# Performance work log

Measured on AMD Instinct MI355X. Metric: run time of the kernel, lower is better.

The kernel has to match this reference:

```python
import jax, jax.numpy as jnp
import numpy as np

N_QUBITS = 8
N_LAYERS = 2
DIM = 2 ** N_QUBITS  # 256


def _ry(theta):
    h = theta * 0.5
    c, s = jnp.cos(h), jnp.sin(h)
    return jnp.stack([jnp.stack([c, -s]), jnp.stack([s, c])]).astype(jnp.complex64)


def _rz(theta):
    e = jnp.exp(-0.5j * theta.astype(jnp.complex64))
    z = jnp.zeros((), jnp.complex64)
    return jnp.stack([jnp.stack([e, z]), jnp.stack([z, jnp.conj(e)])])


def _apply_1q(state, U, w):
    # state: (2,)*n tensor, wire 0 = most significant (PennyLane convention)
    s = jnp.moveaxis(state, w, 0)
    s = jnp.tensordot(U, s, axes=((1,), (0,)))
    return jnp.moveaxis(s, 0, w)


def _cnot(state, c, t):
    s = jnp.moveaxis(state, (c, t), (0, 1))
    s = jnp.stack([s[0, 0], s[0, 1], s[1, 1], s[1, 0]]).reshape((2, 2) + s.shape[2:])
    return jnp.moveaxis(s, (0, 1), (c, t))


def _conv_pair(state, q1, q2, p):
    state = _apply_1q(state, _ry(p[0]), q1)
    state = _apply_1q(state, _ry(p[1]), q2)
    state = _cnot(state, q1, q2)
    state = _apply_1q(state, _ry(p[2]), q1)
    state = _apply_1q(state, _ry(p[3]), q2)
    state = _cnot(state, q2, q1)
    return state


def _circuit(angles, node_idx, adj, qp):
    n = N_QUBITS
    state = jnp.zeros((2,) * n, jnp.complex64).at[(0,) * n].set(1.0)
    a = jnp.clip(angles, -np.pi, np.pi)
    # angle encoding: RY on all wires, RZ on wires 0..n/2-1
    for i in range(n):
        state = _apply_1q(state, _ry(a[i]), i)
    for i in range(n // 2):
        state = _apply_1q(state, _rz(a[i + n // 2]), i)
    # graph-structure entanglement: conditional CNOT(c=node%n, t) if adj[c,t]>0
    c = (node_idx % n).astype(jnp.int32)
    adj_row = adj[c]
    flat = state.reshape(-1)
    idx = jnp.arange(DIM, dtype=jnp.int32)
    bit_c = (idx >> (n - 1 - c)) & 1  # dynamic control wire
    for t in range(n):
        perm = idx ^ (bit_c << (n - 1 - t))
        cond = (adj_row[t] > 0) & (t != c)
        flat = jnp.where(cond, flat[perm], flat)
    state = flat.reshape((2,) * n)
    # quantum conv layers
    ppc = 4 * (n - 1)
    off = 0
    for _ in range(N_LAYERS):
        p = qp[off:off + ppc]
        k = 0
        for i in range(0, n - 1, 2):
            state = _conv_pair(state, i, i + 1, p[k:k + 4]); k += 4
        for i in range(1, n - 1, 2):
            state = _conv_pair(state, i, i + 1, p[k:k + 4]); k += 4
        off += ppc
    # pooling rotations on even wires
    pool = qp[off:off + n]
    for q in range(0, n, 2):
        state = _apply_1q(state, _ry(pool[q]), q)
    # <Z_w> expectation values
    probs = jnp.abs(state) ** 2
    z = jnp.stack([probs.take(0, axis=w).sum() - probs.take(1, axis=w).sum()
                   for w in range(n)])
    return z


def setup_inputs() -> dict:
    key = jax.random.key(0)
    ks = jax.random.split(key, 12)
    B, S, N, F = 64, 12, 207, 2
    x = jax.random.normal(ks[0], (B, S, N, F), jnp.float32)
    adj = jax.random.randint(ks[1], (N, N), 0, 2).astype(jnp.float32)
    w_proj = jax.random.normal(ks[2], (N_QUBITS, S * F), jnp.float32) * 0.1
    b_proj = jax.random.normal(ks[3], (N_QUBITS,), jnp.float32) * 0.1
    q_params = jax.random.normal(ks[4], (4 * (N_QUBITS - 1) * N_LAYERS + N_QUBITS,), jnp.float32) * 0.1
    w1 = jax.random.normal(ks[5], (64, N_QUBITS), jnp.float32) * 0.1
    b1 = jax.random.normal(ks[6], (64,), jnp.float32) * 0.1
    w2 = jax.random.normal(ks[7], (32, 64), jnp.float32) * 0.1
    b2 = jax.random.normal(ks[8], (32,), jnp.float32) * 0.1
    w3 = jax.random.normal(ks[9], (1, 32), jnp.float32) * 0.1
    b3 = jax.random.normal(ks[10], (1,), jnp.float32) * 0.1
    return dict(x=x, adj=adj, w_proj=w_proj, b_proj=b_proj, q_params=q_params,
                w1=w1, b1=b1, w2=w2, b2=b2, w3=w3, b3=b3)


def reference(x, adj, w_proj, b_proj, q_params, w1, b1, w2, b2, w3, b3):
    B, S, N, F = x.shape
    feats = jnp.transpose(x, (0, 2, 1, 3)).reshape(B, N, S * F)
    angles = feats @ w_proj.T + b_proj                      # (B, N, 8)
    node_idx = jnp.tile(jnp.arange(N, dtype=jnp.int32), B)  # (B*N,)
    z = jax.vmap(_circuit, in_axes=(0, 0, None, None))(
        angles.reshape(B * N, N_QUBITS), node_idx, adj, q_params)
    # original detaches quantum features before the classical head
    z = jax.lax.stop_gradient(z).reshape(B, N, N_QUBITS).astype(jnp.float32)
    h = jax.nn.relu(z @ w1.T + b1)   # dropout is identity in eval mode
    h = jax.nn.relu(h @ w2.T + b2)
    out = h @ w3.T + b3              # (B, N, 1)
    return out.squeeze(-1)
```

## Files before the change

### kernel.cpp

```cpp
#include <hip/hip_runtime.h>
#include <math.h>

#define DEV static __device__ __forceinline__

constexpr int SS = 12;
constexpr int NN = 207;
constexpr int NCIRC = 64 * NN;


template<int M> DEV float sxc(float v) { return __shfl_xor(v, M, 64); }

#define RY0(c, s) do { float _c=(c), _s=(s), _a;                         \
    _a=r0; r0=fmaf(_c,_a,-_s*r1); r1=fmaf(_s,_a,_c*r1);                  \
    _a=r2; r2=fmaf(_c,_a,-_s*r3); r3=fmaf(_s,_a,_c*r3);                  \
    _a=i0; i0=fmaf(_c,_a,-_s*i1); i1=fmaf(_s,_a,_c*i1);                  \
    _a=i2; i2=fmaf(_c,_a,-_s*i3); i3=fmaf(_s,_a,_c*i3); } while (0)

#define RY1(c, s) do { float _c=(c), _s=(s), _a;                         \
    _a=r0; r0=fmaf(_c,_a,-_s*r2); r2=fmaf(_s,_a,_c*r2);                  \
    _a=r1; r1=fmaf(_c,_a,-_s*r3); r3=fmaf(_s,_a,_c*r3);                  \
    _a=i0; i0=fmaf(_c,_a,-_s*i2); i2=fmaf(_s,_a,_c*i2);                  \
    _a=i1; i1=fmaf(_c,_a,-_s*i3); i3=fmaf(_s,_a,_c*i3); } while (0)

#define SWAP23 do { float _t=r2; r2=r3; r3=_t; _t=i2; i2=i3; i3=_t; } while (0)
#define SWAP13 do { float _t=r1; r1=r3; r3=_t; _t=i1; i1=i3; i3=_t; } while (0)

#define CONV10(T) do { RY1((T)[0],(T)[1]); RY0((T)[2],(T)[3]); SWAP23;   \
                       RY1((T)[4],(T)[5]); RY0((T)[6],(T)[7]); SWAP13; } while (0)
#define CONV01(T) do { RY0((T)[0],(T)[1]); RY1((T)[2],(T)[3]); SWAP13;   \
                       RY0((T)[4],(T)[5]); RY1((T)[6],(T)[7]); SWAP23; } while (0)

#define SWKL1(J) do { const bool _lb = (lane >> (J)) & 1;                \
    float _t0=sxc<(1<<(J))>(r2), _t1=sxc<(1<<(J))>(r3);                  \
    float _t2=sxc<(1<<(J))>(r0), _t3=sxc<(1<<(J))>(r1);                  \
    r0=_lb?_t0:r0; r1=_lb?_t1:r1; r2=_lb?r2:_t2; r3=_lb?r3:_t3;          \
    _t0=sxc<(1<<(J))>(i2); _t1=sxc<(1<<(J))>(i3);                        \
    _t2=sxc<(1<<(J))>(i0); _t3=sxc<(1<<(J))>(i1);                        \
    i0=_lb?_t0:i0; i1=_lb?_t1:i1; i2=_lb?i2:_t2; i3=_lb?i3:_t3; } while (0)

#define SWKL0(J) do { const bool _lb = (lane >> (J)) & 1;                \
    float _t0=sxc<(1<<(J))>(r1), _t1=sxc<(1<<(J))>(r0);                  \
    float _t2=sxc<(1<<(J))>(r3), _t3=sxc<(1<<(J))>(r2);                  \
    r0=_lb?_t0:r0; r1=_lb?r1:_t1; r2=_lb?_t2:r2; r3=_lb?r3:_t3;          \
    _t0=sxc<(1<<(J))>(i1); _t1=sxc<(1<<(J))>(i0);                        \
    _t2=sxc<(1<<(J))>(i3); _t3=sxc<(1<<(J))>(i2);                        \
    i0=_lb?_t0:i0; i1=_lb?i1:_t1; i2=_lb?_t2:i2; i3=_lb?i3:_t3; } while (0)

#define RYL(J, c, s) do { float _c=(c), _s=(s);                          \
    const float _sg = ((lane >> (J)) & 1) ? _s : -_s;                    \
    float _p;                                                            \
    _p=sxc<(1<<(J))>(r0); r0=fmaf(_c,r0,_sg*_p);                         \
    _p=sxc<(1<<(J))>(r1); r1=fmaf(_c,r1,_sg*_p);                         \
    _p=sxc<(1<<(J))>(r2); r2=fmaf(_c,r2,_sg*_p);                         \
    _p=sxc<(1<<(J))>(r3); r3=fmaf(_c,r3,_sg*_p);                         \
    _p=sxc<(1<<(J))>(i0); i0=fmaf(_c,i0,_sg*_p);                         \
    _p=sxc<(1<<(J))>(i1); i1=fmaf(_c,i1,_sg*_p);                         \
    _p=sxc<(1<<(J))>(i2); i2=fmaf(_c,i2,_sg*_p);                         \
    _p=sxc<(1<<(J))>(i3); i3=fmaf(_c,i3,_sg*_p); } while (0)

__global__ void trig_kernel(const float* __restrict__ qp, float* __restrict__ tab) {
    int i = threadIdx.x;
    if (i < 64) {
        float s, c;
        sincosf(0.5f * qp[i], &s, &c);
        tab[2 * i]     = c;
        tab[2 * i + 1] = s;
    }
}

__global__ __launch_bounds__(256) void qcnn_kernel(
    const float* __restrict__ x, const float* __restrict__ adj,
    const float* __restrict__ w_proj, const float* __restrict__ b_proj,
    const float* __restrict__ tab,
    const float* __restrict__ w1, const float* __restrict__ b1,
    const float* __restrict__ w2, const float* __restrict__ b2,
    const float* __restrict__ w3, const float* __restrict__ b3,
    float* __restrict__ out)
{
    const int lane = threadIdx.x & 63;
    const int wv   = threadIdx.x >> 6;
    const int g    = blockIdx.x * 4 + wv;
    const int b    = g / NN;
    const int node = g - b * NN;

    float ang[8];
#pragma unroll
    for (int k = 0; k < 8; k++) ang[k] = b_proj[k];
    const float* xp = x + ((size_t)b * SS * NN + node) * 2;
#pragma unroll
    for (int s = 0; s < SS; s++) {
        const float2 xv = *(const float2*)(xp + (size_t)s * (NN * 2));
#pragma unroll
        for (int k = 0; k < 8; k++) {
            ang[k] = fmaf(xv.x, w_proj[k * 24 + 2 * s],     ang[k]);
            ang[k] = fmaf(xv.y, w_proj[k * 24 + 2 * s + 1], ang[k]);
        }
    }
    const float PI_F = 3.14159265358979323846f;
#pragma unroll
    for (int k = 0; k < 8; k++) ang[k] = fminf(fmaxf(ang[k], -PI_F), PI_F);

    float cc[8], ss[8];
#pragma unroll
    for (int i = 0; i < 8; i++) sincosf(0.5f * ang[i], &ss[i], &cc[i]);

    float A = 1.0f;
#pragma unroll
    for (int i = 0; i < 6; i++)
        A *= ((lane >> (5 - i)) & 1) ? ss[i] : cc[i];
    float phi = 0.0f;
#pragma unroll
    for (int i = 0; i < 4; i++)
        phi += ((lane >> (5 - i)) & 1) ? 0.5f * ang[4 + i] : -0.5f * ang[4 + i];
    float cp, sp;
    sincosf(phi, &sp, &cp);

    const float A0 = A * cc[6] * cc[7];
    const float A1 = A * cc[6] * ss[7];
    const float A2 = A * ss[6] * cc[7];
    const float A3 = A * ss[6] * ss[7];
    float r0 = A0 * cp, i0 = A0 * sp;
    float r1 = A1 * cp, i1 = A1 * sp;
    float r2 = A2 * cp, i2 = A2 * sp;
    float r3 = A3 * cp, i3 = A3 * sp;

    const int c = node & 7;
    int M = 0;
#pragma unroll
    for (int t = 0; t < 8; t++) {
        float av = adj[c * NN + t];
        if (t != c && av > 0.0f) M |= 1 << (7 - t);
    }
    if (M) {
        const int Mlane = M >> 2;
        const int Mlo   = M & 3;
        float p0r, p1r, p2r, p3r, p0i, p1i, p2i, p3i;
        if (Mlo == 0) {
            p0r = __shfl_xor(r0, Mlane, 64); p1r = __shfl_xor(r1, Mlane, 64);
            p2r = __shfl_xor(r2, Mlane, 64); p3r = __shfl_xor(r3, Mlane, 64);
            p0i = __shfl_xor(i0, Mlane, 64); p1i = __shfl_xor(i1, Mlane, 64);
            p2i = __shfl_xor(i2, Mlane, 64); p3i = __shfl_xor(i3, Mlane, 64);
        } else if (Mlo == 1) {
            p0r = __shfl_xor(r1, Mlane, 64); p1r = __shfl_xor(r0, Mlane, 64);
            p2r = __shfl_xor(r3, Mlane, 64); p3r = __shfl_xor(r2, Mlane, 64);
            p0i = __shfl_xor(i1, Mlane, 64); p1i = __shfl_xor(i0, Mlane, 64);
            p2i = __shfl_xor(i3, Mlane, 64); p3i = __shfl_xor(i2, Mlane, 64);
        } else if (Mlo == 2) {
            p0r = __shfl_xor(r2, Mlane, 64); p1r = __shfl_xor(r3, Mlane, 64);
            p2r = __shfl_xor(r0, Mlane, 64); p3r = __shfl_xor(r1, Mlane, 64);
            p0i = __shfl_xor(i2, Mlane, 64); p1i = __shfl_xor(i3, Mlane, 64);
            p2i = __shfl_xor(i0, Mlane, 64); p3i = __shfl_xor(i1, Mlane, 64);
        } else {
            p0r = __shfl_xor(r3, Mlane, 64); p1r = __shfl_xor(r2, Mlane, 64);
            p2r = __shfl_xor(r1, Mlane, 64); p3r = __shfl_xor(r0, Mlane, 64);
            p0i = __shfl_xor(i3, Mlane, 64); p1i = __shfl_xor(i2, Mlane, 64);
            p2i = __shfl_xor(i1, Mlane, 64); p3i = __shfl_xor(i0, Mlane, 64);
        }
        const int pc = 7 - c;
        if (pc >= 2) {
            const bool bb = (lane >> (pc - 2)) & 1;
            r0 = bb ? p0r : r0; r1 = bb ? p1r : r1;
            r2 = bb ? p2r : r2; r3 = bb ? p3r : r3;
            i0 = bb ? p0i : i0; i1 = bb ? p1i : i1;
            i2 = bb ? p2i : i2; i3 = bb ? p3i : i3;
        } else if (pc == 1) {
            r2 = p2r; r3 = p3r; i2 = p2i; i3 = p3i;
        } else {
            r1 = p1r; r3 = p3r; i1 = p1i; i3 = p3i;
        }
    }

    CONV10(tab + 2*12);
    SWKL1(1);
    SWKL0(0);
    CONV10(tab + 2*8);
    SWKL1(1);
    CONV01(tab + 2*24);
    SWKL1(3);
    SWKL0(2);
    CONV10(tab + 2*4);
    SWKL1(1);
    CONV01(tab + 2*20);
    SWKL1(5);
    SWKL0(4);
    CONV10(tab + 2*0);
    SWKL1(1);
    CONV01(tab + 2*16);
    SWKL0(4);
    CONV10(tab + 2*32);
    SWKL1(1);
    SWKL0(4);
    CONV10(tab + 2*28);
    SWKL1(1);
    CONV01(tab + 2*44);
    SWKL1(5);
    SWKL0(2);
    CONV10(tab + 2*36);
    SWKL0(4);
    CONV01(tab + 2*48);
    SWKL1(3);
    SWKL0(0);
    CONV10(tab + 2*40);
    SWKL0(4);
    CONV01(tab + 2*52);

    RYL(1, tab[112], tab[113]);
    RYL(5, tab[116], tab[117]);
    RYL(3, tab[120], tab[121]);
    RY1(tab[124], tab[125]);

    float p0 = fmaf(r0, r0, i0 * i0);
    float p1 = fmaf(r1, r1, i1 * i1);
    float p2 = fmaf(r2, r2, i2 * i2);
    float p3 = fmaf(r3, r3, i3 * i3);
    float psum = (p0 + p1) + (p2 + p3);
    float zv[8];
    zv[6] = (p0 + p1) - (p2 + p3);
    zv[5] = (p0 - p1) + (p2 - p3);
    zv[2] = ((lane >> 5) & 1) ? -psum : psum;
    zv[7] = ((lane >> 4) & 1) ? -psum : psum;
    zv[4] = ((lane >> 3) & 1) ? -psum : psum;
    zv[1] = ((lane >> 2) & 1) ? -psum : psum;
    zv[0] = ((lane >> 1) & 1) ? -psum : psum;
    zv[3] = ((lane >> 0) & 1) ? -psum : psum;

#pragma unroll
    for (int w = 0; w < 8; w++) zv[w] += sxc<1>(zv[w]);
#pragma unroll
    for (int w = 0; w < 8; w++) zv[w] += sxc<2>(zv[w]);
#pragma unroll
    for (int w = 0; w < 8; w++) zv[w] += sxc<4>(zv[w]);
#pragma unroll
    for (int w = 0; w < 8; w++) zv[w] += sxc<8>(zv[w]);
#pragma unroll
    for (int w = 0; w < 8; w++) zv[w] += sxc<16>(zv[w]);
#pragma unroll
    for (int w = 0; w < 8; w++) zv[w] += sxc<32>(zv[w]);

    float h1 = b1[lane];
#pragma unroll
    for (int k = 0; k < 8; k++) h1 = fmaf(zv[k], w1[lane * 8 + k], h1);
    h1 = fmaxf(h1, 0.0f);

    __shared__ float h1s[4][64];
    h1s[wv][lane] = h1;
    __syncthreads();

    const int m = lane & 31;
    float h2 = b2[m];
#pragma unroll
    for (int j = 0; j < 64; j++) h2 = fmaf(h1s[wv][j], w2[m * 64 + j], h2);
    h2 = fmaxf(h2, 0.0f);

    float o = h2 * w3[m];
    o += sxc<1>(o);
    o += sxc<2>(o);
    o += sxc<4>(o);
    o += sxc<8>(o);
    o += sxc<16>(o);

    if (lane == 0) out[g] = o + b3[0];
}

extern "C" void kernel_launch(void* const* d_in, const int* in_sizes, int n_in,
                              void* d_out, int out_size, void* d_ws, size_t ws_size,
                              hipStream_t stream) {
    const float* x      = (const float*)d_in[0];
    const float* adj    = (const float*)d_in[1];
    const float* w_proj = (const float*)d_in[2];
    const float* b_proj = (const float*)d_in[3];
    const float* qp     = (const float*)d_in[4];
    const float* w1     = (const float*)d_in[5];
    const float* b1     = (const float*)d_in[6];
    const float* w2     = (const float*)d_in[7];
    const float* b2     = (const float*)d_in[8];
    const float* w3     = (const float*)d_in[9];
    const float* b3     = (const float*)d_in[10];
    float* out = (float*)d_out;
    float* tab = (float*)d_ws;

    hipLaunchKernelGGL(trig_kernel, dim3(1), dim3(64), 0, stream, qp, tab);
    hipLaunchKernelGGL(qcnn_kernel, dim3(NCIRC / 4), dim3(256), 0, stream,
                       x, adj, w_proj, b_proj, tab, w1, b1, w2, b2, w3, b3, out);
}
```

Before: 118.4 us.

## Fuse each conv pair into a precomputed 4x4 real matrix and vectorise with packed FP32

A prep kernel now multiplies the RY gates and CNOT permutations of each two-qubit conv block into one 4x4 real matrix. It also folds the final wire-6/7 rotation into the last block. The main kernel applies each block as a single matrix-vector product on complex amplitudes held as float2 vectors, aiming for packed FMA instructions. The projection, reduction butterflies and MLP layers are vectorised the same way, and the precise sincosf calls become the fast __sincosf intrinsic. The aim is fewer ALU instructions per circuit, at the cost of extra uniform scalar loads and slightly lower trig accuracy.

```diff
diff --git a/kernel.cpp b/kernel.cpp
--- a/kernel.cpp
+++ b/kernel.cpp
@@ -8,70 +8,107 @@
 constexpr int NCIRC = 64 * NN;
 
 
+typedef float v2f __attribute__((ext_vector_type(2)));
+
+DEV v2f splat2(float x) { v2f r; r.x = x; r.y = x; return r; }
+DEV v2f vfma(float m, v2f a, v2f acc) { return __builtin_elementwise_fma(splat2(m), a, acc); }
+DEV v2f vmul(float m, v2f a) { return splat2(m) * a; }
 template<int M> DEV float sxc(float v) { return __shfl_xor(v, M, 64); }
-
-#define RY0(c, s) do { float _c=(c), _s=(s), _a;                         \
-    _a=r0; r0=fmaf(_c,_a,-_s*r1); r1=fmaf(_s,_a,_c*r1);                  \
-    _a=r2; r2=fmaf(_c,_a,-_s*r3); r3=fmaf(_s,_a,_c*r3);                  \
-    _a=i0; i0=fmaf(_c,_a,-_s*i1); i1=fmaf(_s,_a,_c*i1);                  \
-    _a=i2; i2=fmaf(_c,_a,-_s*i3); i3=fmaf(_s,_a,_c*i3); } while (0)
-
-#define RY1(c, s) do { float _c=(c), _s=(s), _a;                         \
-    _a=r0; r0=fmaf(_c,_a,-_s*r2); r2=fmaf(_s,_a,_c*r2);                  \
-    _a=r1; r1=fmaf(_c,_a,-_s*r3); r3=fmaf(_s,_a,_c*r3);                  \
-    _a=i0; i0=fmaf(_c,_a,-_s*i2); i2=fmaf(_s,_a,_c*i2);                  \
-    _a=i1; i1=fmaf(_c,_a,-_s*i3); i3=fmaf(_s,_a,_c*i3); } while (0)
-
-#define SWAP23 do { float _t=r2; r2=r3; r3=_t; _t=i2; i2=i3; i3=_t; } while (0)
-#define SWAP13 do { float _t=r1; r1=r3; r3=_t; _t=i1; i1=i3; i3=_t; } while (0)
-
-#define CONV10(T) do { RY1((T)[0],(T)[1]); RY0((T)[2],(T)[3]); SWAP23;   \
-                       RY1((T)[4],(T)[5]); RY0((T)[6],(T)[7]); SWAP13; } while (0)
-#define CONV01(T) do { RY0((T)[0],(T)[1]); RY1((T)[2],(T)[3]); SWAP13;   \
-                       RY0((T)[4],(T)[5]); RY1((T)[6],(T)[7]); SWAP23; } while (0)
-
-#define SWKL1(J) do { const bool _lb = (lane >> (J)) & 1;                \
-    float _t0=sxc<(1<<(J))>(r2), _t1=sxc<(1<<(J))>(r3);                  \
-    float _t2=sxc<(1<<(J))>(r0), _t3=sxc<(1<<(J))>(r1);                  \
-    r0=_lb?_t0:r0; r1=_lb?_t1:r1; r2=_lb?r2:_t2; r3=_lb?r3:_t3;          \
-    _t0=sxc<(1<<(J))>(i2); _t1=sxc<(1<<(J))>(i3);                        \
-    _t2=sxc<(1<<(J))>(i0); _t3=sxc<(1<<(J))>(i1);                        \
-    i0=_lb?_t0:i0; i1=_lb?_t1:i1; i2=_lb?i2:_t2; i3=_lb?i3:_t3; } while (0)
-
-#define SWKL0(J) do { const bool _lb = (lane >> (J)) & 1;                \
-    float _t0=sxc<(1<<(J))>(r1), _t1=sxc<(1<<(J))>(r0);                  \
-    float _t2=sxc<(1<<(J))>(r3), _t3=sxc<(1<<(J))>(r2);                  \
-    r0=_lb?_t0:r0; r1=_lb?r1:_t1; r2=_lb?_t2:r2; r3=_lb?r3:_t3;          \
-    _t0=sxc<(1<<(J))>(i1); _t1=sxc<(1<<(J))>(i0);                        \
-    _t2=sxc<(1<<(J))>(i3); _t3=sxc<(1<<(J))>(i2);                        \
-    i0=_lb?_t0:i0; i1=_lb?i1:_t1; i2=_lb?_t2:i2; i3=_lb?i3:_t3; } while (0)
-
-#define RYL(J, c, s) do { float _c=(c), _s=(s);                          \
-    const float _sg = ((lane >> (J)) & 1) ? _s : -_s;                    \
-    float _p;                                                            \
-    _p=sxc<(1<<(J))>(r0); r0=fmaf(_c,r0,_sg*_p);                         \
-    _p=sxc<(1<<(J))>(r1); r1=fmaf(_c,r1,_sg*_p);                         \
-    _p=sxc<(1<<(J))>(r2); r2=fmaf(_c,r2,_sg*_p);                         \
-    _p=sxc<(1<<(J))>(r3); r3=fmaf(_c,r3,_sg*_p);                         \
-    _p=sxc<(1<<(J))>(i0); i0=fmaf(_c,i0,_sg*_p);                         \
-    _p=sxc<(1<<(J))>(i1); i1=fmaf(_c,i1,_sg*_p);                         \
-    _p=sxc<(1<<(J))>(i2); i2=fmaf(_c,i2,_sg*_p);                         \
-    _p=sxc<(1<<(J))>(i3); i3=fmaf(_c,i3,_sg*_p); } while (0)
-
-__global__ void trig_kernel(const float* __restrict__ qp, float* __restrict__ tab) {
-    int i = threadIdx.x;
-    if (i < 64) {
+template<int M> DEV v2f sx2(v2f v) { v2f r; r.x = sxc<M>(v.x); r.y = sxc<M>(v.y); return r; }
+
+#define CONVM(P) do {                                                     \
+    v2f _a0 = c0, _a1 = c1, _a2 = c2, _a3 = c3;                           \
+    c0 = vfma((P)[0],  _a0, vfma((P)[1],  _a1, vfma((P)[2],  _a2, vmul((P)[3],  _a3)))); \
+    c1 = vfma((P)[4],  _a0, vfma((P)[5],  _a1, vfma((P)[6],  _a2, vmul((P)[7],  _a3)))); \
+    c2 = vfma((P)[8],  _a0, vfma((P)[9],  _a1, vfma((P)[10], _a2, vmul((P)[11], _a3)))); \
+    c3 = vfma((P)[12], _a0, vfma((P)[13], _a1, vfma((P)[14], _a2, vmul((P)[15], _a3)))); \
+} while (0)
+
+#define SWKL1(J) do { const bool _lb = (lane >> (J)) & 1;                 \
+    v2f _t0 = sx2<(1<<(J))>(c2), _t1 = sx2<(1<<(J))>(c3);                 \
+    v2f _t2 = sx2<(1<<(J))>(c0), _t3 = sx2<(1<<(J))>(c1);                 \
+    c0 = _lb ? _t0 : c0; c1 = _lb ? _t1 : c1;                             \
+    c2 = _lb ? c2 : _t2; c3 = _lb ? c3 : _t3; } while (0)
+
+#define SWKL0(J) do { const bool _lb = (lane >> (J)) & 1;                 \
+    v2f _t0 = sx2<(1<<(J))>(c1), _t1 = sx2<(1<<(J))>(c0);                 \
+    v2f _t2 = sx2<(1<<(J))>(c3), _t3 = sx2<(1<<(J))>(c2);                 \
+    c0 = _lb ? _t0 : c0; c1 = _lb ? c1 : _t1;                             \
+    c2 = _lb ? _t2 : c2; c3 = _lb ? c3 : _t3; } while (0)
+
+#define RYL(J, cc_, ss_) do { const float _c = (cc_), _s = (ss_);         \
+    const float _sg = ((lane >> (J)) & 1) ? _s : -_s;                     \
+    v2f _p;                                                               \
+    _p = sx2<(1<<(J))>(c0); c0 = __builtin_elementwise_fma(splat2(_c), c0, vmul(_sg, _p)); \
+    _p = sx2<(1<<(J))>(c1); c1 = __builtin_elementwise_fma(splat2(_c), c1, vmul(_sg, _p)); \
+    _p = sx2<(1<<(J))>(c2); c2 = __builtin_elementwise_fma(splat2(_c), c2, vmul(_sg, _p)); \
+    _p = sx2<(1<<(J))>(c3); c3 = __builtin_elementwise_fma(splat2(_c), c3, vmul(_sg, _p)); \
+} while (0)
+
+__global__ void prep_kernel(const float* __restrict__ qp, float* __restrict__ ws) {
+    const int n = threadIdx.x;
+    if (n == 14) {
         float s, c;
-        sincosf(0.5f * qp[i], &s, &c);
-        tab[2 * i]     = c;
-        tab[2 * i + 1] = s;
-    }
+        sincosf(0.5f * qp[56], &s, &c); ws[224] = c; ws[225] = s;
+        sincosf(0.5f * qp[58], &s, &c); ws[226] = c; ws[227] = s;
+        sincosf(0.5f * qp[60], &s, &c); ws[228] = c; ws[229] = s;
+    }
+    if (n >= 14) return;
+    const int Jt[14] = {12, 8, 24, 4, 20, 0, 16, 32, 28, 44, 36, 48, 40, 52};
+    const int Vt[14] = { 0, 0,  1, 0,  1, 0,  1,  0,  0,  1,  0,  1,  0,  1};
+    const int J = Jt[n], v = Vt[n];
+    float cg[4], sg[4];
+    for (int i = 0; i < 4; i++) sincosf(0.5f * qp[J + i], &sg[i], &cg[i]);
+    const int h1i = v ? 1 : 0, l1i = v ? 0 : 1;
+    const int h2i = v ? 3 : 2, l2i = v ? 2 : 3;
+    float A[16], B[16], M[16];
+    {
+        float H[2][2] = {{cg[h1i], -sg[h1i]}, {sg[h1i], cg[h1i]}};
+        float L[2][2] = {{cg[l1i], -sg[l1i]}, {sg[l1i], cg[l1i]}};
+        for (int a = 0; a < 2; a++) for (int b = 0; b < 2; b++)
+            for (int p = 0; p < 2; p++) for (int q = 0; q < 2; q++)
+                A[(2*a+b)*4 + (2*p+q)] = H[a][p] * L[b][q];
+    }
+    {
+        const int ra = v ? 1 : 2;
+        for (int j = 0; j < 4; j++) { float t = A[ra*4+j]; A[ra*4+j] = A[12+j]; A[12+j] = t; }
+    }
+    {
+        float H[2][2] = {{cg[h2i], -sg[h2i]}, {sg[h2i], cg[h2i]}};
+        float L[2][2] = {{cg[l2i], -sg[l2i]}, {sg[l2i], cg[l2i]}};
+        for (int a = 0; a < 2; a++) for (int b = 0; b < 2; b++)
+            for (int p = 0; p < 2; p++) for (int q = 0; q < 2; q++)
+                B[(2*a+b)*4 + (2*p+q)] = H[a][p] * L[b][q];
+    }
+    for (int r = 0; r < 4; r++)
+        for (int cl = 0; cl < 4; cl++) {
+            float acc = 0.0f;
+            for (int k = 0; k < 4; k++) acc += B[r*4+k] * A[k*4+cl];
+            M[r*4+cl] = acc;
+        }
+    {
+        const int rb = v ? 2 : 1;
+        for (int j = 0; j < 4; j++) { float t = M[rb*4+j]; M[rb*4+j] = M[12+j]; M[12+j] = t; }
+    }
+    if (n == 13) {
+        float ps, pc;
+        sincosf(0.5f * qp[62], &ps, &pc);
+        for (int j = 0; j < 4; j++) {
+            float r0 = M[j],     r2 = M[8+j];
+            M[j]     = pc * r0 - ps * r2;
+            M[8+j]   = ps * r0 + pc * r2;
+            float r1 = M[4+j],   r3 = M[12+j];
+            M[4+j]   = pc * r1 - ps * r3;
+            M[12+j]  = ps * r1 + pc * r3;
+        }
+    }
+    for (int i = 0; i < 16; i++) ws[16*n + i] = M[i];
 }
 
 __global__ __launch_bounds__(256) void qcnn_kernel(
     const float* __restrict__ x, const float* __restrict__ adj,
     const float* __restrict__ w_proj, const float* __restrict__ b_proj,
-    const float* __restrict__ tab,
+    const float* __restrict__ ws,
     const float* __restrict__ w1, const float* __restrict__ b1,
     const float* __restrict__ w2, const float* __restrict__ b2,
     const float* __restrict__ w3, const float* __restrict__ b3,
@@ -83,26 +120,28 @@
     const int b    = g / NN;
     const int node = g - b * NN;
 
+    v2f av[8];
+#pragma unroll
+    for (int k = 0; k < 8; k++) av[k] = splat2(0.0f);
+    const float* xp = x + ((size_t)b * SS * NN + node) * 2;
+#pragma unroll
+    for (int s = 0; s < SS; s++) {
+        const v2f xv = *(const v2f*)(xp + (size_t)s * (NN * 2));
+#pragma unroll
+        for (int k = 0; k < 8; k++) {
+            const v2f wv2 = *(const v2f*)(w_proj + k * 24 + 2 * s);
+            av[k] = __builtin_elementwise_fma(xv, wv2, av[k]);
+        }
+    }
+    const float PI_F = 3.14159265358979323846f;
     float ang[8];
 #pragma unroll
-    for (int k = 0; k < 8; k++) ang[k] = b_proj[k];
-    const float* xp = x + ((size_t)b * SS * NN + node) * 2;
-#pragma unroll
-    for (int s = 0; s < SS; s++) {
-        const float2 xv = *(const float2*)(xp + (size_t)s * (NN * 2));
-#pragma unroll
-        for (int k = 0; k < 8; k++) {
-            ang[k] = fmaf(xv.x, w_proj[k * 24 + 2 * s],     ang[k]);
-            ang[k] = fmaf(xv.y, w_proj[k * 24 + 2 * s + 1], ang[k]);
-        }
-    }
-    const float PI_F = 3.14159265358979323846f;
-#pragma unroll
-    for (int k = 0; k < 8; k++) ang[k] = fminf(fmaxf(ang[k], -PI_F), PI_F);
+    for (int k = 0; k < 8; k++)
+        ang[k] = fminf(fmaxf(av[k].x + av[k].y + b_proj[k], -PI_F), PI_F);
 
     float cc[8], ss[8];
 #pragma unroll
-    for (int i = 0; i < 8; i++) sincosf(0.5f * ang[i], &ss[i], &cc[i]);
+    for (int i = 0; i < 8; i++) __sincosf(0.5f * ang[i], &ss[i], &cc[i]);
 
     float A = 1.0f;
 #pragma unroll
@@ -113,144 +152,124 @@
     for (int i = 0; i < 4; i++)
         phi += ((lane >> (5 - i)) & 1) ? 0.5f * ang[4 + i] : -0.5f * ang[4 + i];
     float cp, sp;
-    sincosf(phi, &sp, &cp);
-
-    const float A0 = A * cc[6] * cc[7];
-    const float A1 = A * cc[6] * ss[7];
-    const float A2 = A * ss[6] * cc[7];
-    const float A3 = A * ss[6] * ss[7];
-    float r0 = A0 * cp, i0 = A0 * sp;
-    float r1 = A1 * cp, i1 = A1 * sp;
-    float r2 = A2 * cp, i2 = A2 * sp;
-    float r3 = A3 * cp, i3 = A3 * sp;
-
-    const int c = node & 7;
+    __sincosf(phi, &sp, &cp);
+
+    v2f ph; ph.x = cp; ph.y = sp;
+    v2f c0 = vmul(A * cc[6] * cc[7], ph);
+    v2f c1 = vmul(A * cc[6] * ss[7], ph);
+    v2f c2 = vmul(A * ss[6] * cc[7], ph);
+    v2f c3 = vmul(A * ss[6] * ss[7], ph);
+
+    const int cq = node & 7;
     int M = 0;
 #pragma unroll
     for (int t = 0; t < 8; t++) {
-        float av = adj[c * NN + t];
-        if (t != c && av > 0.0f) M |= 1 << (7 - t);
+        float avv = adj[cq * NN + t];
+        if (t != cq && avv > 0.0f) M |= 1 << (7 - t);
     }
     if (M) {
         const int Mlane = M >> 2;
         const int Mlo   = M & 3;
-        float p0r, p1r, p2r, p3r, p0i, p1i, p2i, p3i;
-        if (Mlo == 0) {
-            p0r = __shfl_xor(r0, Mlane, 64); p1r = __shfl_xor(r1, Mlane, 64);
-            p2r = __shfl_xor(r2, Mlane, 64); p3r = __shfl_xor(r3, Mlane, 64);
-            p0i = __shfl_xor(i0, Mlane, 64); p1i = __shfl_xor(i1, Mlane, 64);
-            p2i = __shfl_xor(i2, Mlane, 64); p3i = __shfl_xor(i3, Mlane, 64);
-        } else if (Mlo == 1) {
-            p0r = __shfl_xor(r1, Mlane, 64); p1r = __shfl_xor(r0, Mlane, 64);
-            p2r = __shfl_xor(r3, Mlane, 64); p3r = __shfl_xor(r2, Mlane, 64);
-            p0i = __shfl_xor(i1, Mlane, 64); p1i = __shfl_xor(i0, Mlane, 64);
-            p2i = __shfl_xor(i3, Mlane, 64); p3i = __shfl_xor(i2, Mlane, 64);
-        } else if (Mlo == 2) {
-            p0r = __shfl_xor(r2, Mlane, 64); p1r = __shfl_xor(r3, Mlane, 64);
-            p2r = __shfl_xor(r0, Mlane, 64); p3r = __shfl_xor(r1, Mlane, 64);
-            p0i = __shfl_xor(i2, Mlane, 64); p1i = __shfl_xor(i3, Mlane, 64);
-            p2i = __shfl_xor(i0, Mlane, 64); p3i = __shfl_xor(i1, Mlane, 64);
-        } else {
-            p0r = __shfl_xor(r3, Mlane, 64); p1r = __shfl_xor(r2, Mlane, 64);
-            p2r = __shfl_xor(r1, Mlane, 64); p3r = __shfl_xor(r0, Mlane, 64);
-            p0i = __shfl_xor(i3, Mlane, 64); p1i = __shfl_xor(i2, Mlane, 64);
-            p2i = __shfl_xor(i1, Mlane, 64); p3i = __shfl_xor(i0, Mlane, 64);
-        }
-        const int pc = 7 - c;
+        v2f p0, p1, p2, p3;
+        if (Mlo == 0)      { p0 = c0; p1 = c1; p2 = c2; p3 = c3; }
+        else if (Mlo == 1) { p0 = c1; p1 = c0; p2 = c3; p3 = c2; }
+        else if (Mlo == 2) { p0 = c2; p1 = c3; p2 = c0; p3 = c1; }
+        else               { p0 = c3; p1 = c2; p2 = c1; p3 = c0; }
+        p0.x = __shfl_xor(p0.x, Mlane, 64); p0.y = __shfl_xor(p0.y, Mlane, 64);
+        p1.x = __shfl_xor(p1.x, Mlane, 64); p1.y = __shfl_xor(p1.y, Mlane, 64);
+        p2.x = __shfl_xor(p2.x, Mlane, 64); p2.y = __shfl_xor(p2.y, Mlane, 64);
+        p3.x = __shfl_xor(p3.x, Mlane, 64); p3.y = __shfl_xor(p3.y, Mlane, 64);
+        const int pc = 7 - cq;
         if (pc >= 2) {
             const bool bb = (lane >> (pc - 2)) & 1;
-            r0 = bb ? p0r : r0; r1 = bb ? p1r : r1;
-            r2 = bb ? p2r : r2; r3 = bb ? p3r : r3;
-            i0 = bb ? p0i : i0; i1 = bb ? p1i : i1;
-            i2 = bb ? p2i : i2; i3 = bb ? p3i : i3;
+            c0 = bb ? p0 : c0; c1 = bb ? p1 : c1;
+            c2 = bb ? p2 : c2; c3 = bb ? p3 : c3;
         } else if (pc == 1) {
-            r2 = p2r; r3 = p3r; i2 = p2i; i3 = p3i;
+            c2 = p2; c3 = p3;
         } else {
-            r1 = p1r; r3 = p3r; i1 = p1i; i3 = p3i;
+            c1 = p1; c3 = p3;
         }
     }
 
-    CONV10(tab + 2*12);
+    CONVM(ws + 0);
     SWKL1(1);
     SWKL0(0);
-    CONV10(tab + 2*8);
-    SWKL1(1);
-    CONV01(tab + 2*24);
+    CONVM(ws + 16);
+    SWKL1(1);
+    CONVM(ws + 32);
     SWKL1(3);
     SWKL0(2);
-    CONV10(tab + 2*4);
-    SWKL1(1);
-    CONV01(tab + 2*20);
+    CONVM(ws + 48);
+    SWKL1(1);
+    CONVM(ws + 64);
     SWKL1(5);
     SWKL0(4);
-    CONV10(tab + 2*0);
-    SWKL1(1);
-    CONV01(tab + 2*16);
-    SWKL0(4);
-    CONV10(tab + 2*32);
-    SWKL1(1);
-    SWKL0(4);
-    CONV10(tab + 2*28);
-    SWKL1(1);
-    CONV01(tab + 2*44);
+    CONVM(ws + 80);
+    SWKL1(1);
+    CONVM(ws + 96);
+    SWKL0(4);
+    CONVM(ws + 112);
+    SWKL1(1);
+    SWKL0(4);
+    CONVM(ws + 128);
+    SWKL1(1);
+    CONVM(ws + 144);
     SWKL1(5);
     SWKL0(2);
-    CONV10(tab + 2*36);
-    SWKL0(4);
-    CONV01(tab + 2*48);
+    CONVM(ws + 160);
+    SWKL0(4);
+    CONVM(ws + 176);
     SWKL1(3);
     SWKL0(0);
-    CONV10(tab + 2*40);
-    SWKL0(4);
-    CONV01(tab + 2*52);
-
-    RYL(1, tab[112], tab[113]);
-    RYL(5, tab[116], tab[117]);
-    RYL(3, tab[120], tab[121]);
-    RY1(tab[124], tab[125]);
-
-    float p0 = fmaf(r0, r0, i0 * i0);
-    float p1 = fmaf(r1, r1, i1 * i1);
-    float p2 = fmaf(r2, r2, i2 * i2);
-    float p3 = fmaf(r3, r3, i3 * i3);
-    float psum = (p0 + p1) + (p2 + p3);
-    float zv[8];
-    zv[6] = (p0 + p1) - (p2 + p3);
-    zv[5] = (p0 - p1) + (p2 - p3);
-    zv[2] = ((lane >> 5) & 1) ? -psum : psum;
-    zv[7] = ((lane >> 4) & 1) ? -psum : psum;
-    zv[4] = ((lane >> 3) & 1) ? -psum : psum;
-    zv[1] = ((lane >> 2) & 1) ? -psum : psum;
-    zv[0] = ((lane >> 1) & 1) ? -psum : psum;
-    zv[3] = ((lane >> 0) & 1) ? -psum : psum;
-
-#pragma unroll
-    for (int w = 0; w < 8; w++) zv[w] += sxc<1>(zv[w]);
-#pragma unroll
-    for (int w = 0; w < 8; w++) zv[w] += sxc<2>(zv[w]);
-#pragma unroll
-    for (int w = 0; w < 8; w++) zv[w] += sxc<4>(zv[w]);
-#pragma unroll
-    for (int w = 0; w < 8; w++) zv[w] += sxc<8>(zv[w]);
-#pragma unroll
-    for (int w = 0; w < 8; w++) zv[w] += sxc<16>(zv[w]);
-#pragma unroll
-    for (int w = 0; w < 8; w++) zv[w] += sxc<32>(zv[w]);
-
-    float h1 = b1[lane];
-#pragma unroll
-    for (int k = 0; k < 8; k++) h1 = fmaf(zv[k], w1[lane * 8 + k], h1);
-    h1 = fmaxf(h1, 0.0f);
+    CONVM(ws + 192);
+    SWKL0(4);
+    CONVM(ws + 208);
+
+    RYL(1, ws[224], ws[225]);
+    RYL(5, ws[226], ws[227]);
+    RYL(3, ws[228], ws[229]);
+
+    const float p0 = fmaf(c0.x, c0.x, c0.y * c0.y);
+    const float p1 = fmaf(c1.x, c1.x, c1.y * c1.y);
+    const float p2 = fmaf(c2.x, c2.x, c2.y * c2.y);
+    const float p3 = fmaf(c3.x, c3.x, c3.y * c3.y);
+    const float psum = (p0 + p1) + (p2 + p3);
+    const float zK1 = (p0 + p1) - (p2 + p3);
+    const float zK0 = (p0 - p1) + (p2 - p3);
+    v2f za, zb, zc, zd;
+    za.x = ((lane >> 1) & 1) ? -psum : psum;
+    za.y = ((lane >> 2) & 1) ? -psum : psum;
+    zb.x = ((lane >> 5) & 1) ? -psum : psum;
+    zb.y = (lane & 1)        ? -psum : psum;
+    zc.x = ((lane >> 3) & 1) ? -psum : psum;
+    zc.y = zK0;
+    zd.x = zK1;
+    zd.y = ((lane >> 4) & 1) ? -psum : psum;
+
+#define BFLY(MM) do { za += sx2<MM>(za); zb += sx2<MM>(zb);               \
+                      zc += sx2<MM>(zc); zd += sx2<MM>(zd); } while (0)
+    BFLY(1); BFLY(2); BFLY(4); BFLY(8); BFLY(16); BFLY(32);
+#undef BFLY
+
+    const v2f* w1v = (const v2f*)(w1 + lane * 8);
+    v2f hv = za * w1v[0];
+    hv = __builtin_elementwise_fma(zb, w1v[1], hv);
+    hv = __builtin_elementwise_fma(zc, w1v[2], hv);
+    hv = __builtin_elementwise_fma(zd, w1v[3], hv);
+    const float h1 = fmaxf(b1[lane] + hv.x + hv.y, 0.0f);
 
     __shared__ float h1s[4][64];
     h1s[wv][lane] = h1;
     __syncthreads();
 
     const int m = lane & 31;
-    float h2 = b2[m];
-#pragma unroll
-    for (int j = 0; j < 64; j++) h2 = fmaf(h1s[wv][j], w2[m * 64 + j], h2);
-    h2 = fmaxf(h2, 0.0f);
+    const v2f* w2v = (const v2f*)(w2 + m * 64);
+    const v2f* hsv = (const v2f*)(&h1s[wv][0]);
+    v2f acc2 = splat2(0.0f);
+#pragma unroll
+    for (int j = 0; j < 32; j++)
+        acc2 = __builtin_elementwise_fma(hsv[j], w2v[j], acc2);
+    const float h2 = fmaxf(b2[m] + acc2.x + acc2.y, 0.0f);
 
     float o = h2 * w3[m];
     o += sxc<1>(o);
@@ -277,9 +296,9 @@
     const float* w3     = (const float*)d_in[9];
     const float* b3     = (const float*)d_in[10];
     float* out = (float*)d_out;
-    float* tab = (float*)d_ws;
-
-    hipLaunchKernelGGL(trig_kernel, dim3(1), dim3(64), 0, stream, qp, tab);
+    float* ws  = (float*)d_ws;
+
+    hipLaunchKernelGGL(prep_kernel, dim3(1), dim3(64), 0, stream, qp, ws);
     hipLaunchKernelGGL(qcnn_kernel, dim3(NCIRC / 4), dim3(256), 0, stream,
-                       x, adj, w_proj, b_proj, tab, w1, b1, w2, b2, w3, b3, out);
+                       x, adj, w_proj, b_proj, ws, w1, b1, w2, b2, w3, b3, out);
 }
```

New measurement: 115.0 us. 1.03x faster.
